# Kernel tuning notes

Measured on AMD Instinct MI355X. Metric: run time of the kernel, lower is better.

## Reference

```python
import jax, jax.numpy as jnp
import numpy as np

N_NODES = 100000
N_EDGES = 1600000
DIM = 128
N_GRAPHS = 64
N_LAYERS = 7
LEAKY_SLOPE = 0.01
BN_EPS = 1e-5


def setup_inputs() -> dict:
    key = jax.random.key(0)
    ks = jax.random.split(key, 6)
    x = jax.random.normal(ks[0], (N_NODES, DIM), dtype=jnp.float32)
    edge_index = jax.random.randint(ks[1], (2, N_EDGES), 0, N_NODES, dtype=jnp.int64)
    batch = jnp.sort(jax.random.randint(ks[2], (N_NODES,), 0, N_GRAPHS, dtype=jnp.int64))
    # GCNConv weights (Glorot-ish scale), biases, BatchNorm affine params
    Ws = jax.random.normal(ks[3], (N_LAYERS, DIM, DIM), dtype=jnp.float32) * (1.0 / np.sqrt(DIM))
    bs = jnp.zeros((N_LAYERS, DIM), dtype=jnp.float32)
    gammas = jnp.ones((N_LAYERS, DIM), dtype=jnp.float32)
    betas = jnp.zeros((N_LAYERS, DIM), dtype=jnp.float32)
    return {"x": x, "edge_index": edge_index, "batch": batch,
            "Ws": Ws, "bs": bs, "gammas": gammas, "betas": betas}


def reference(x, edge_index, batch, Ws, bs, gammas, betas):
    N = x.shape[0]
    # Add self-loops once (shared by all 7 GCNConv layers)
    loops = jnp.arange(N, dtype=edge_index.dtype)
    src = jnp.concatenate([edge_index[0], loops])  # [E+N]
    dst = jnp.concatenate([edge_index[1], loops])  # [E+N]
    # Symmetric normalization: deg over destination (incl. self-loops)
    deg = jax.ops.segment_sum(jnp.ones_like(dst, dtype=x.dtype), dst, num_segments=N)
    dinv = jax.lax.rsqrt(jnp.maximum(deg, 1.0))  # deg >= 1 from self-loops
    norm = dinv[src] * dinv[dst]                 # [E+N]

    def block(h, W, b, gamma, beta):
        # GCNConv: linear -> gather -> normalized scatter-add
        h = h @ W + b                                            # [N, D]
        msgs = h[src] * norm[:, None]                            # [E+N, D]
        h = jax.ops.segment_sum(msgs, dst, num_segments=N)       # [N, D]
        # LeakyReLU then BatchNorm (batch statistics over nodes)
        h = jax.nn.leaky_relu(h, negative_slope=LEAKY_SLOPE)
        mu = jnp.mean(h, axis=0)
        var = jnp.mean((h - mu) ** 2, axis=0)
        h = (h - mu) * jax.lax.rsqrt(var + BN_EPS) * gamma + beta
        return h

    h = x
    for i in range(N_LAYERS):
        h = block(h, Ws[i], bs[i], gammas[i], betas[i])

    # global_mean_pool over graph ids
    sums = jax.ops.segment_sum(h, batch, num_segments=N_GRAPHS)          # [G, D]
    cnt = jax.ops.segment_sum(jnp.ones((N,), h.dtype), batch, num_segments=N_GRAPHS)
    return sums / jnp.maximum(cnt, 1.0)[:, None]
```

## Files before the change

kernel.cpp:

```cpp
#include <hip/hip_runtime.h>
#include <hip/hip_fp16.h>

#define DIMM 128
#define LEAKY_S 0.01f
#define EPS_BN 1e-5f

typedef _Float16 half8 __attribute__((ext_vector_type(8)));
typedef float f32x4 __attribute__((ext_vector_type(4)));


__global__ __launch_bounds__(256) void k_deg(const int* __restrict__ dst, int* __restrict__ deg, int E, int N) {
    int i = blockIdx.x * 256 + threadIdx.x;
    if (i < E) {
        int d = dst[i];
        if ((unsigned)d < (unsigned)N) atomicAdd(&deg[d], 1);
    }
}

__global__ __launch_bounds__(256) void k_dinv(const int* __restrict__ deg, float* __restrict__ dinv, int N) {
    int i = blockIdx.x * 256 + threadIdx.x;
    if (i < N) dinv[i] = rsqrtf((float)(deg[i] + 1));
}

__global__ __launch_bounds__(256) void k_scanA(const int* __restrict__ deg, int* __restrict__ bsum, int n) {
    __shared__ int ws[4];
    int tid = threadIdx.x, lane = tid & 63, wid = tid >> 6;
    int base = blockIdx.x * 1024;
    int s = 0;
    #pragma unroll
    for (int j = 0; j < 4; ++j) {
        int i = base + j * 256 + tid;
        if (i < n) s += deg[i];
    }
    #pragma unroll
    for (int off = 32; off > 0; off >>= 1) s += __shfl_down(s, (unsigned)off, 64);
    if (lane == 0) ws[wid] = s;
    __syncthreads();
    if (tid == 0) bsum[blockIdx.x] = ws[0] + ws[1] + ws[2] + ws[3];
}

__global__ __launch_bounds__(64) void k_scanB(const int* __restrict__ bsum, int* __restrict__ bofs,
                                              int* __restrict__ rowptr, int nb, int n) {
    if (threadIdx.x == 0) {
        int run = 0;
        for (int j = 0; j < nb; ++j) { bofs[j] = run; run += bsum[j]; }
        rowptr[n] = run;
    }
}

__global__ __launch_bounds__(1024) void k_scanC(const int* __restrict__ deg, const int* __restrict__ bofs,
                                                int* __restrict__ rowptr, int n) {
    __shared__ int wsum[16];
    int tid = threadIdx.x, lane = tid & 63, wid = tid >> 6;
    int i = blockIdx.x * 1024 + tid;
    int v = (i < n) ? deg[i] : 0;
    int s = v;
    #pragma unroll
    for (int off = 1; off < 64; off <<= 1) {
        int t = __shfl_up(s, (unsigned)off, 64);
        if (lane >= off) s += t;
    }
    if (lane == 63) wsum[wid] = s;
    __syncthreads();
    if (wid == 0 && lane < 16) {
        int ws = wsum[lane];
        #pragma unroll
        for (int off = 1; off < 16; off <<= 1) {
            int t = __shfl_up(ws, (unsigned)off, 64);
            if (lane >= off) ws += t;
        }
        wsum[lane] = ws;
    }
    __syncthreads();
    int woff = wid ? wsum[wid - 1] : 0;
    if (i < n) rowptr[i] = bofs[blockIdx.x] + woff + (s - v);
}

__global__ __launch_bounds__(256) void k_fill(const int* __restrict__ src, const int* __restrict__ dst,
                                              const int* __restrict__ rowptr, int* __restrict__ cursor,
                                              const float* __restrict__ dinv,
                                              int2* __restrict__ csr, int E, int N) {
    int i = blockIdx.x * 256 + threadIdx.x;
    if (i < E) {
        int d = dst[i], s = src[i];
        if ((unsigned)d < (unsigned)N && (unsigned)s < (unsigned)N) {
            int pos = atomicAdd(&cursor[d], 1);
            int idx = rowptr[d] + pos;
            csr[idx] = make_int2(s, __float_as_int(dinv[s] * dinv[d]));
        }
    }
}


__global__ __launch_bounds__(256) void k_wprep(const float* __restrict__ Ws, __half* __restrict__ Wt) {
    int l = blockIdx.y;
    int i = blockIdx.x * 256 + threadIdx.x;
    int n = i >> 7, k = i & 127;
    Wt[(size_t)l * DIMM * DIMM + n * DIMM + k] = __float2half(Ws[(size_t)l * DIMM * DIMM + k * DIMM + n]);
}


__global__ __launch_bounds__(256) void k_gemm(const void* __restrict__ A, const __half* __restrict__ Wt,
                                              const float* __restrict__ bias, const float* __restrict__ ss,
                                              __half* __restrict__ out, int N, int a_half) {
    __shared__ char smem[128 * 272];
    int tid = threadIdx.x;
    int lane = tid & 63, wid = tid >> 6;
    int quad = lane >> 4, lm = lane & 15;
    int row0 = blockIdx.x * 128;

    {
        int seg = tid & 31;
        int col = seg * 4;
        float4 sc = *(const float4*)(ss + col);
        float4 sh = *(const float4*)(ss + 128 + col);
        const float*  Af = (const float*)A;
        const __half* Ah = (const __half*)A;
        for (int i = tid; i < 128 * 32; i += 256) {
            int r = i >> 5;
            int gr = row0 + r;
            float4 v = make_float4(0.f, 0.f, 0.f, 0.f);
            if (gr < N) {
                if (a_half) {
                    union { uint2 u; __half2 h2[2]; } ld;
                    ld.u = *(const uint2*)(Ah + (size_t)gr * DIMM + col);
                    float2 f0 = __half22float2(ld.h2[0]);
                    float2 f1 = __half22float2(ld.h2[1]);
                    v = make_float4(f0.x, f0.y, f1.x, f1.y);
                } else {
                    v = *(const float4*)(Af + (size_t)gr * DIMM + col);
                }
                v.x = v.x * sc.x + sh.x; v.y = v.y * sc.y + sh.y;
                v.z = v.z * sc.z + sh.z; v.w = v.w * sc.w + sh.w;
            }
            union { _Float16 h[4]; uint2 u; } pk;
            pk.h[0] = (_Float16)v.x; pk.h[1] = (_Float16)v.y;
            pk.h[2] = (_Float16)v.z; pk.h[3] = (_Float16)v.w;
            *(uint2*)(smem + r * 272 + seg * 8) = pk.u;
        }
    }

    f32x4 acc[2][8];
    #pragma unroll
    for (int c = 0; c < 8; ++c) {
        float bc = bias[c * 16 + lm];
        acc[0][c] = (f32x4){bc, bc, bc, bc};
        acc[1][c] = acc[0][c];
    }
    __syncthreads();

    const _Float16* Wt16 = (const _Float16*)Wt;
    #pragma unroll
    for (int kc = 0; kc < 4; ++kc) {
        half8 a0 = *(const half8*)(smem + (wid * 32 + lm) * 272 + kc * 64 + quad * 16);
        half8 a1 = *(const half8*)(smem + (wid * 32 + 16 + lm) * 272 + kc * 64 + quad * 16);
        #pragma unroll
        for (int c = 0; c < 8; ++c) {
            half8 b = *(const half8*)(Wt16 + (c * 16 + lm) * DIMM + kc * 32 + quad * 8);
            acc[0][c] = __builtin_amdgcn_mfma_f32_16x16x32_f16(a0, b, acc[0][c], 0, 0, 0);
            acc[1][c] = __builtin_amdgcn_mfma_f32_16x16x32_f16(a1, b, acc[1][c], 0, 0, 0);
        }
    }

    __syncthreads();
    #pragma unroll
    for (int r = 0; r < 2; ++r)
        #pragma unroll
        for (int c = 0; c < 8; ++c)
            #pragma unroll
            for (int i = 0; i < 4; ++i) {
                int rit = wid * 32 + r * 16 + quad * 4 + i;
                int col = c * 16 + lm;
                *(_Float16*)(smem + rit * 256 + col * 2) = (_Float16)acc[r][c][i];
            }
    __syncthreads();
    for (int i = tid; i < 128 * 16; i += 256) {
        int r = i >> 4, seg = i & 15;
        int gr = row0 + r;
        if (gr < N)
            ((uint4*)(out + (size_t)gr * DIMM))[seg] = ((const uint4*)(smem + r * 256))[seg];
    }
}


__global__ __launch_bounds__(256) void k_agg(const __half* __restrict__ t, __half* __restrict__ out,
                                             const int* __restrict__ rowptr, const int2* __restrict__ csr,
                                             const float* __restrict__ dinv,
                                             float* __restrict__ stats, int N, int nwaves) {
    int tid = threadIdx.x;
    int lane = tid & 63, wid = tid >> 6;
    int grp = lane >> 4;
    int l16 = lane & 15;
    int gw = blockIdx.x * 4 + wid;

    float sx[8] = {0.f, 0.f, 0.f, 0.f, 0.f, 0.f, 0.f, 0.f};
    float qx[8] = {0.f, 0.f, 0.f, 0.f, 0.f, 0.f, 0.f, 0.f};

    for (int node = gw; node < N; node += nwaves) {
        float di = dinv[node];
        float sn = di * di;
        float v[8] = {0.f, 0.f, 0.f, 0.f, 0.f, 0.f, 0.f, 0.f};
        if (grp == 0) {
            union { half8 h; __half2 h2[4]; } u;
            u.h = *(const half8*)(t + (size_t)node * DIMM + l16 * 8);
            #pragma unroll
            for (int p = 0; p < 4; ++p) {
                float2 f = __half22float2(u.h2[p]);
                v[2 * p]     = sn * f.x;
                v[2 * p + 1] = sn * f.y;
            }
        }
        int e = rowptr[node], e1 = rowptr[node + 1];
        for (; e + 16 <= e1; e += 16) {
            #pragma unroll
            for (int j = 0; j < 4; ++j) {
                int2 cw = csr[e + 4 * j + grp];
                float wgt = __int_as_float(cw.y);
                union { half8 h; __half2 h2[4]; } u;
                u.h = *(const half8*)(t + (size_t)cw.x * DIMM + l16 * 8);
                #pragma unroll
                for (int p = 0; p < 4; ++p) {
                    float2 f = __half22float2(u.h2[p]);
                    v[2 * p]     = fmaf(wgt, f.x, v[2 * p]);
                    v[2 * p + 1] = fmaf(wgt, f.y, v[2 * p + 1]);
                }
            }
        }
        if (e < e1) {
            #pragma unroll
            for (int j = 0; j < 4; ++j) {
                int idx = e + 4 * j + grp;
                if (idx < e1) {
                    int2 cw = csr[idx];
                    float wgt = __int_as_float(cw.y);
                    union { half8 h; __half2 h2[4]; } u;
                    u.h = *(const half8*)(t + (size_t)cw.x * DIMM + l16 * 8);
                    #pragma unroll
                    for (int p = 0; p < 4; ++p) {
                        float2 f = __half22float2(u.h2[p]);
                        v[2 * p]     = fmaf(wgt, f.x, v[2 * p]);
                        v[2 * p + 1] = fmaf(wgt, f.y, v[2 * p + 1]);
                    }
                }
            }
        }
        #pragma unroll
        for (int i = 0; i < 8; ++i) {
            v[i] += __shfl_down(v[i], 32, 64);
            v[i] += __shfl_down(v[i], 16, 64);
        }
        if (grp == 0) {
            union { _Float16 h[8]; uint4 u4; } pk;
            #pragma unroll
            for (int i = 0; i < 8; ++i) {
                v[i] = v[i] > 0.f ? v[i] : LEAKY_S * v[i];
                sx[i] += v[i];
                qx[i] += v[i] * v[i];
                pk.h[i] = (_Float16)v[i];
            }
            *(uint4*)(out + (size_t)node * DIMM + l16 * 8) = pk.u4;
        }
    }

    __shared__ float red[4 * 128];
    if (grp == 0) {
        *(float4*)(red + wid * 128 + l16 * 8)     = make_float4(sx[0], sx[1], sx[2], sx[3]);
        *(float4*)(red + wid * 128 + l16 * 8 + 4) = make_float4(sx[4], sx[5], sx[6], sx[7]);
    }
    __syncthreads();
    if (tid < 128) {
        float s = red[tid] + red[128 + tid] + red[256 + tid] + red[384 + tid];
        atomicAdd(&stats[tid], s);
    }
    __syncthreads();
    if (grp == 0) {
        *(float4*)(red + wid * 128 + l16 * 8)     = make_float4(qx[0], qx[1], qx[2], qx[3]);
        *(float4*)(red + wid * 128 + l16 * 8 + 4) = make_float4(qx[4], qx[5], qx[6], qx[7]);
    }
    __syncthreads();
    if (tid < 128) {
        float s = red[tid] + red[128 + tid] + red[256 + tid] + red[384 + tid];
        atomicAdd(&stats[128 + tid], s);
    }
}

__global__ __launch_bounds__(128) void k_bnfin(const float* __restrict__ stats, const float* __restrict__ gamma,
                                               const float* __restrict__ beta, float* __restrict__ ss_out,
                                               float inv_n) {
    int c = threadIdx.x;
    float mu  = stats[c] * inv_n;
    float var = stats[128 + c] * inv_n - mu * mu;
    float a = gamma[c] * rsqrtf(var + EPS_BN);
    ss_out[c]       = a;
    ss_out[128 + c] = beta[c] - mu * a;
}

__global__ __launch_bounds__(128) void k_init_ss(float* __restrict__ ss) {
    int c = threadIdx.x;
    ss[c] = 1.0f;
    ss[128 + c] = 0.0f;
}


__global__ __launch_bounds__(64) void k_cnt_bs(const int* __restrict__ batch, int* __restrict__ cnt, int N, int G) {
    int g = blockIdx.x * 64 + threadIdx.x;
    if (g >= G) return;
    int lo = 0, hi = N;
    while (lo < hi) { int mid = (lo + hi) >> 1; if (batch[mid] < g) lo = mid + 1; else hi = mid; }
    int lb = lo;
    lo = 0; hi = N;
    while (lo < hi) { int mid = (lo + hi) >> 1; if (batch[mid] <= g) lo = mid + 1; else hi = mid; }
    cnt[g] = lo - lb;
}

__global__ __launch_bounds__(128) void k_pool(const __half* __restrict__ h, const int* __restrict__ batch,
                                              float* __restrict__ pool, int N, int G) {
    const int CHUNK = 128;
    int start = blockIdx.x * CHUNK;
    if (start >= N) return;
    int end = min(start + CHUNK, N);
    int tid = threadIdx.x;
    float acc = 0.f;
    int cur = batch[start];
    for (int n = start; n < end; ++n) {
        int g = batch[n];
        if (g != cur) {
            if ((unsigned)cur < (unsigned)G) atomicAdd(&pool[(size_t)cur * DIMM + tid], acc);
            acc = 0.f; cur = g;
        }
        acc += __half2float(h[(size_t)n * DIMM + tid]);
    }
    if ((unsigned)cur < (unsigned)G) atomicAdd(&pool[(size_t)cur * DIMM + tid], acc);
}

__global__ __launch_bounds__(256) void k_poolfin(const float* __restrict__ pool, const int* __restrict__ cnt,
                                                 const float* __restrict__ ss, float* __restrict__ out, int G) {
    int idx = blockIdx.x * 256 + threadIdx.x;
    if (idx < G * DIMM) {
        int g = idx >> 7, c = idx & 127;
        float m = pool[idx] / (float)max(cnt[g], 1);
        out[idx] = ss[c] * m + ss[128 + c];
    }
}


extern "C" void kernel_launch(void* const* d_in, const int* in_sizes, int n_in,
                              void* d_out, int out_size, void* d_ws, size_t ws_size,
                              hipStream_t stream) {
    const float* x      = (const float*)d_in[0];
    const int*   ei     = (const int*)d_in[1];
    const int*   batch  = (const int*)d_in[2];
    const float* Ws     = (const float*)d_in[3];
    const float* bs     = (const float*)d_in[4];
    const float* gammas = (const float*)d_in[5];
    const float* betas  = (const float*)d_in[6];
    float* outp = (float*)d_out;

    int N = in_sizes[2];
    int E = in_sizes[1] / 2;
    int L = in_sizes[3] / (DIMM * DIMM);
    int G = out_size / DIMM;

    const int* srcv = ei;
    const int* dstv = ei + E;

    int nb = (N + 1023) / 1024;

    char* w = (char*)d_ws;
    auto alloc = [&](size_t bytes) { char* p = w; w += (bytes + 511) & ~size_t(511); return p; };
    int*    deg    = (int*)   alloc((size_t)N * 4);
    int*    cursor = (int*)   alloc((size_t)N * 4);
    int*    rowptr = (int*)   alloc((size_t)(N + 1) * 4);
    int*    bsum   = (int*)   alloc((size_t)nb * 4);
    int*    bofs   = (int*)   alloc((size_t)nb * 4);
    int2*   csr    = (int2*)  alloc((size_t)E * 8);
    float*  dinv   = (float*) alloc((size_t)N * 4);
    __half* hA     = (__half*)alloc((size_t)N * DIMM * 2);
    __half* hB     = (__half*)alloc((size_t)N * DIMM * 2);
    __half* Wt     = (__half*)alloc((size_t)L * DIMM * DIMM * 2);
    float*  stats  = (float*) alloc((size_t)L * 256 * 4);
    float*  ss     = (float*) alloc((size_t)(L + 1) * 256 * 4);
    float*  pool   = (float*) alloc((size_t)G * DIMM * 4);
    int*    cnt    = (int*)   alloc((size_t)G * 4);

    hipMemsetAsync(deg,    0, (size_t)N * 4, stream);
    hipMemsetAsync(cursor, 0, (size_t)N * 4, stream);
    hipMemsetAsync(stats,  0, (size_t)L * 256 * 4, stream);
    hipMemsetAsync(pool,   0, (size_t)G * DIMM * 4, stream);

    k_init_ss<<<1, 128, 0, stream>>>(ss);
    k_wprep<<<dim3(64, L), 256, 0, stream>>>(Ws, Wt);
    k_deg  <<<(E + 255) / 256, 256, 0, stream>>>(dstv, deg, E, N);
    k_dinv <<<(N + 255) / 256, 256, 0, stream>>>(deg, dinv, N);
    k_scanA<<<nb, 256, 0, stream>>>(deg, bsum, N);
    k_scanB<<<1, 64, 0, stream>>>(bsum, bofs, rowptr, nb, N);
    k_scanC<<<nb, 1024, 0, stream>>>(deg, bofs, rowptr, N);
    k_fill <<<(E + 255) / 256, 256, 0, stream>>>(srcv, dstv, rowptr, cursor, dinv, csr, E, N);

    const void* cur_in = (const void*)x;
    int a_half = 0;
    for (int l = 0; l < L; ++l) {
        k_gemm<<<(N + 127) / 128, 256, 0, stream>>>(cur_in, Wt + (size_t)l * DIMM * DIMM,
                                                    bs + (size_t)l * DIMM, ss + (size_t)l * 256, hA, N, a_half);
        const int nblk = 2048;
        k_agg<<<nblk, 256, 0, stream>>>(hA, hB, rowptr, csr, dinv,
                                        stats + (size_t)l * 256, N, nblk * 4);
        k_bnfin<<<1, 128, 0, stream>>>(stats + (size_t)l * 256, gammas + (size_t)l * DIMM,
                                       betas + (size_t)l * DIMM, ss + (size_t)(l + 1) * 256, 1.0f / (float)N);
        cur_in = (const void*)hB;
        a_half = 1;
    }

    k_cnt_bs<<<(G + 63) / 64, 64, 0, stream>>>(batch, cnt, N, G);
    k_pool<<<(N + 127) / 128, 128, 0, stream>>>(hB, batch, pool, N, G);
    k_poolfin<<<(G * DIMM + 255) / 256, 256, 0, stream>>>(pool, cnt, ss + (size_t)L * 256, outp, G);
}
```

Baseline: 1.288 ms.

## Slice GEMM output into feature-column planes and aggregate per slice with compact CSR

```diff
diff --git a/kernel.cpp b/kernel.cpp
--- a/kernel.cpp
+++ b/kernel.cpp
@@ -4,9 +4,11 @@
 #define DIMM 128
 #define LEAKY_S 0.01f
 #define EPS_BN 1e-5f
+#define NSLICE 8
 
 typedef _Float16 half8 __attribute__((ext_vector_type(8)));
 typedef float f32x4 __attribute__((ext_vector_type(4)));
+typedef unsigned int uivec4 __attribute__((ext_vector_type(4)));
 
 
 __global__ __launch_bounds__(256) void k_deg(const int* __restrict__ dst, int* __restrict__ deg, int E, int N) {
@@ -17,11 +19,6 @@
     }
 }
 
-__global__ __launch_bounds__(256) void k_dinv(const int* __restrict__ deg, float* __restrict__ dinv, int N) {
-    int i = blockIdx.x * 256 + threadIdx.x;
-    if (i < N) dinv[i] = rsqrtf((float)(deg[i] + 1));
-}
-
 __global__ __launch_bounds__(256) void k_scanA(const int* __restrict__ deg, int* __restrict__ bsum, int n) {
     __shared__ int ws[4];
     int tid = threadIdx.x, lane = tid & 63, wid = tid >> 6;
@@ -30,7 +27,7 @@
     #pragma unroll
     for (int j = 0; j < 4; ++j) {
         int i = base + j * 256 + tid;
-        if (i < n) s += deg[i];
+        if (i < n) s += deg[i] + 1;
     }
     #pragma unroll
     for (int off = 32; off > 0; off >>= 1) s += __shfl_down(s, (unsigned)off, 64);
@@ -53,7 +50,7 @@
     __shared__ int wsum[16];
     int tid = threadIdx.x, lane = tid & 63, wid = tid >> 6;
     int i = blockIdx.x * 1024 + tid;
-    int v = (i < n) ? deg[i] : 0;
+    int v = (i < n) ? deg[i] + 1 : 0;
     int s = v;
     #pragma unroll
     for (int off = 1; off < 64; off <<= 1) {
@@ -76,17 +73,24 @@
     if (i < n) rowptr[i] = bofs[blockIdx.x] + woff + (s - v);
 }
 
+__global__ __launch_bounds__(256) void k_dinvself(const int* __restrict__ deg, const int* __restrict__ rowptr,
+                                                  float* __restrict__ dinv, int* __restrict__ csrcol, int N) {
+    int i = blockIdx.x * 256 + threadIdx.x;
+    if (i < N) {
+        dinv[i] = rsqrtf((float)(deg[i] + 1));
+        csrcol[rowptr[i]] = i;
+    }
+}
+
 __global__ __launch_bounds__(256) void k_fill(const int* __restrict__ src, const int* __restrict__ dst,
                                               const int* __restrict__ rowptr, int* __restrict__ cursor,
-                                              const float* __restrict__ dinv,
-                                              int2* __restrict__ csr, int E, int N) {
+                                              int* __restrict__ csrcol, int E, int N) {
     int i = blockIdx.x * 256 + threadIdx.x;
     if (i < E) {
         int d = dst[i], s = src[i];
         if ((unsigned)d < (unsigned)N && (unsigned)s < (unsigned)N) {
-            int pos = atomicAdd(&cursor[d], 1);
-            int idx = rowptr[d] + pos;
-            csr[idx] = make_int2(s, __float_as_int(dinv[s] * dinv[d]));
+            int pos = 1 + atomicAdd(&cursor[d], 1);
+            csrcol[rowptr[d] + pos] = s;
         }
     }
 }
@@ -174,113 +178,109 @@
                 *(_Float16*)(smem + rit * 256 + col * 2) = (_Float16)acc[r][c][i];
             }
     __syncthreads();
-    for (int i = tid; i < 128 * 16; i += 256) {
-        int r = i >> 4, seg = i & 15;
+    {
+        int r = tid & 127, h = tid >> 7;
         int gr = row0 + r;
-        if (gr < N)
-            ((uint4*)(out + (size_t)gr * DIMM))[seg] = ((const uint4*)(smem + r * 256))[seg];
-    }
-}
-
+        if (gr < N) {
+            #pragma unroll
+            for (int s = 0; s < NSLICE; ++s) {
+                uivec4 val = *(const uivec4*)(smem + r * 256 + s * 32 + h * 16);
+                *(uivec4*)((char*)out + ((size_t)s * N + gr) * 32 + h * 16) = val;
+            }
+        }
+    }
+}
+
+
+__device__ __forceinline__ void h8acc(const __half* p, float w, float* v) {
+    union { uivec4 u; __half2 h2[4]; } ld;
+    ld.u = *(const uivec4*)p;
+    #pragma unroll
+    for (int q = 0; q < 4; ++q) {
+        float2 f = __half22float2(ld.h2[q]);
+        v[2 * q]     = fmaf(w, f.x, v[2 * q]);
+        v[2 * q + 1] = fmaf(w, f.y, v[2 * q + 1]);
+    }
+}
 
 __global__ __launch_bounds__(256) void k_agg(const __half* __restrict__ t, __half* __restrict__ out,
-                                             const int* __restrict__ rowptr, const int2* __restrict__ csr,
+                                             const int* __restrict__ rowptr, const int* __restrict__ csr,
                                              const float* __restrict__ dinv,
-                                             float* __restrict__ stats, int N, int nwaves) {
+                                             float* __restrict__ stats, int N, int stride) {
     int tid = threadIdx.x;
     int lane = tid & 63, wid = tid >> 6;
-    int grp = lane >> 4;
-    int l16 = lane & 15;
-    int gw = blockIdx.x * 4 + wid;
-
-    float sx[8] = {0.f, 0.f, 0.f, 0.f, 0.f, 0.f, 0.f, 0.f};
-    float qx[8] = {0.f, 0.f, 0.f, 0.f, 0.f, 0.f, 0.f, 0.f};
-
-    for (int node = gw; node < N; node += nwaves) {
-        float di = dinv[node];
-        float sn = di * di;
-        float v[8] = {0.f, 0.f, 0.f, 0.f, 0.f, 0.f, 0.f, 0.f};
-        if (grp == 0) {
-            union { half8 h; __half2 h2[4]; } u;
-            u.h = *(const half8*)(t + (size_t)node * DIMM + l16 * 8);
-            #pragma unroll
-            for (int p = 0; p < 4; ++p) {
-                float2 f = __half22float2(u.h2[p]);
-                v[2 * p]     = sn * f.x;
-                v[2 * p + 1] = sn * f.y;
+    int pr = lane >> 1;
+    int half = lane & 1;
+    int s = blockIdx.x & 7;
+    int bs = blockIdx.x >> 3;
+    int gp = bs * 128 + wid * 32 + pr;
+
+    const __half* ts = t + (size_t)s * N * 16;
+
+    float sx[8] = {0.f,0.f,0.f,0.f,0.f,0.f,0.f,0.f};
+    float qx[8] = {0.f,0.f,0.f,0.f,0.f,0.f,0.f,0.f};
+    float acc[8] = {0.f,0.f,0.f,0.f,0.f,0.f,0.f,0.f};
+
+    int node = gp;
+    int e = 0, eend = 0;
+    float dn = 0.f;
+    if (node < N) { e = rowptr[node]; eend = rowptr[node + 1]; dn = dinv[node]; }
+
+    for (;;) {
+        bool act = (node < N);
+        if (__ballot(act) == 0ull) break;
+        int e0 = e;
+        #pragma unroll
+        for (int k = 0; k < 4; ++k) {
+            bool st = act && (e0 + k < eend);
+            if (st) {
+                int col = __builtin_nontemporal_load(csr + e0 + k);
+                float w = dinv[col] * dn;
+                h8acc(ts + (size_t)col * 16 + half * 8, w, acc);
             }
         }
-        int e = rowptr[node], e1 = rowptr[node + 1];
-        for (; e + 16 <= e1; e += 16) {
-            #pragma unroll
-            for (int j = 0; j < 4; ++j) {
-                int2 cw = csr[e + 4 * j + grp];
-                float wgt = __int_as_float(cw.y);
-                union { half8 h; __half2 h2[4]; } u;
-                u.h = *(const half8*)(t + (size_t)cw.x * DIMM + l16 * 8);
+        if (act) {
+            e = min(e0 + 4, eend);
+            if (e >= eend) {
+                union { _Float16 h[8]; uivec4 u4; } pk;
                 #pragma unroll
-                for (int p = 0; p < 4; ++p) {
-                    float2 f = __half22float2(u.h2[p]);
-                    v[2 * p]     = fmaf(wgt, f.x, v[2 * p]);
-                    v[2 * p + 1] = fmaf(wgt, f.y, v[2 * p + 1]);
+                for (int i = 0; i < 8; ++i) {
+                    float v = acc[i];
+                    v = v > 0.f ? v : LEAKY_S * v;
+                    sx[i] += v;
+                    qx[i] += v * v;
+                    pk.h[i] = (_Float16)v;
+                    acc[i] = 0.f;
                 }
+                __builtin_nontemporal_store(pk.u4,
+                    (uivec4*)(out + (size_t)node * DIMM + s * 16 + half * 8));
+                node += stride;
+                if (node < N) { e = rowptr[node]; eend = rowptr[node + 1]; dn = dinv[node]; }
             }
         }
-        if (e < e1) {
-            #pragma unroll
-            for (int j = 0; j < 4; ++j) {
-                int idx = e + 4 * j + grp;
-                if (idx < e1) {
-                    int2 cw = csr[idx];
-                    float wgt = __int_as_float(cw.y);
-                    union { half8 h; __half2 h2[4]; } u;
-                    u.h = *(const half8*)(t + (size_t)cw.x * DIMM + l16 * 8);
-                    #pragma unroll
-                    for (int p = 0; p < 4; ++p) {
-                        float2 f = __half22float2(u.h2[p]);
-                        v[2 * p]     = fmaf(wgt, f.x, v[2 * p]);
-                        v[2 * p + 1] = fmaf(wgt, f.y, v[2 * p + 1]);
-                    }
-                }
-            }
-        }
+    }
+
+    #pragma unroll
+    for (int i = 0; i < 8; ++i) {
+        #pragma unroll
+        for (int d = 2; d <= 32; d <<= 1) {
+            sx[i] += __shfl_down(sx[i], (unsigned)d, 64);
+            qx[i] += __shfl_down(qx[i], (unsigned)d, 64);
+        }
+    }
+    __shared__ float red[4][32];
+    if (lane < 2) {
         #pragma unroll
         for (int i = 0; i < 8; ++i) {
-            v[i] += __shfl_down(v[i], 32, 64);
-            v[i] += __shfl_down(v[i], 16, 64);
-        }
-        if (grp == 0) {
-            union { _Float16 h[8]; uint4 u4; } pk;
-            #pragma unroll
-            for (int i = 0; i < 8; ++i) {
-                v[i] = v[i] > 0.f ? v[i] : LEAKY_S * v[i];
-                sx[i] += v[i];
-                qx[i] += v[i] * v[i];
-                pk.h[i] = (_Float16)v[i];
-            }
-            *(uint4*)(out + (size_t)node * DIMM + l16 * 8) = pk.u4;
-        }
-    }
-
-    __shared__ float red[4 * 128];
-    if (grp == 0) {
-        *(float4*)(red + wid * 128 + l16 * 8)     = make_float4(sx[0], sx[1], sx[2], sx[3]);
-        *(float4*)(red + wid * 128 + l16 * 8 + 4) = make_float4(sx[4], sx[5], sx[6], sx[7]);
-    }
-    __syncthreads();
-    if (tid < 128) {
-        float s = red[tid] + red[128 + tid] + red[256 + tid] + red[384 + tid];
-        atomicAdd(&stats[tid], s);
-    }
-    __syncthreads();
-    if (grp == 0) {
-        *(float4*)(red + wid * 128 + l16 * 8)     = make_float4(qx[0], qx[1], qx[2], qx[3]);
-        *(float4*)(red + wid * 128 + l16 * 8 + 4) = make_float4(qx[4], qx[5], qx[6], qx[7]);
-    }
-    __syncthreads();
-    if (tid < 128) {
-        float s = red[tid] + red[128 + tid] + red[256 + tid] + red[384 + tid];
-        atomicAdd(&stats[128 + tid], s);
+            red[wid][half * 8 + i]      = sx[i];
+            red[wid][16 + half * 8 + i] = qx[i];
+        }
+    }
+    __syncthreads();
+    if (tid < 32) {
+        float v = red[0][tid] + red[1][tid] + red[2][tid] + red[3][tid];
+        int gc = s * 16 + (tid & 15);
+        atomicAdd(&stats[(tid < 16 ? 0 : 128) + gc], v);
     }
 }
 
@@ -373,7 +373,7 @@
     int*    rowptr = (int*)   alloc((size_t)(N + 1) * 4);
     int*    bsum   = (int*)   alloc((size_t)nb * 4);
     int*    bofs   = (int*)   alloc((size_t)nb * 4);
-    int2*   csr    = (int2*)  alloc((size_t)E * 8);
+    int*    csrcol = (int*)   alloc((size_t)(E + N) * 4);
     float*  dinv   = (float*) alloc((size_t)N * 4);
     __half* hA     = (__half*)alloc((size_t)N * DIMM * 2);
     __half* hB     = (__half*)alloc((size_t)N * DIMM * 2);
@@ -383,28 +383,30 @@
     float*  pool   = (float*) alloc((size_t)G * DIMM * 4);
     int*    cnt    = (int*)   alloc((size_t)G * 4);
 
-    hipMemsetAsync(deg,    0, (size_t)N * 4, stream);
-    hipMemsetAsync(cursor, 0, (size_t)N * 4, stream);
-    hipMemsetAsync(stats,  0, (size_t)L * 256 * 4, stream);
-    hipMemsetAsync(pool,   0, (size_t)G * DIMM * 4, stream);
+    (void)hipMemsetAsync(deg,    0, (size_t)N * 4, stream);
+    (void)hipMemsetAsync(cursor, 0, (size_t)N * 4, stream);
+    (void)hipMemsetAsync(stats,  0, (size_t)L * 256 * 4, stream);
+    (void)hipMemsetAsync(pool,   0, (size_t)G * DIMM * 4, stream);
 
     k_init_ss<<<1, 128, 0, stream>>>(ss);
     k_wprep<<<dim3(64, L), 256, 0, stream>>>(Ws, Wt);
     k_deg  <<<(E + 255) / 256, 256, 0, stream>>>(dstv, deg, E, N);
-    k_dinv <<<(N + 255) / 256, 256, 0, stream>>>(deg, dinv, N);
     k_scanA<<<nb, 256, 0, stream>>>(deg, bsum, N);
     k_scanB<<<1, 64, 0, stream>>>(bsum, bofs, rowptr, nb, N);
     k_scanC<<<nb, 1024, 0, stream>>>(deg, bofs, rowptr, N);
-    k_fill <<<(E + 255) / 256, 256, 0, stream>>>(srcv, dstv, rowptr, cursor, dinv, csr, E, N);
+    k_dinvself<<<(N + 255) / 256, 256, 0, stream>>>(deg, rowptr, dinv, csrcol, N);
+    k_fill <<<(E + 255) / 256, 256, 0, stream>>>(srcv, dstv, rowptr, cursor, csrcol, E, N);
+
+    const int nblk = 2048;
+    const int stride = (nblk / NSLICE) * 128;
 
     const void* cur_in = (const void*)x;
     int a_half = 0;
     for (int l = 0; l < L; ++l) {
         k_gemm<<<(N + 127) / 128, 256, 0, stream>>>(cur_in, Wt + (size_t)l * DIMM * DIMM,
                                                     bs + (size_t)l * DIMM, ss + (size_t)l * 256, hA, N, a_half);
-        const int nblk = 2048;
-        k_agg<<<nblk, 256, 0, stream>>>(hA, hB, rowptr, csr, dinv,
-                                        stats + (size_t)l * 256, N, nblk * 4);
+        k_agg<<<nblk, 256, 0, stream>>>(hA, hB, rowptr, csrcol, dinv,
+                                        stats + (size_t)l * 256, N, stride);
         k_bnfin<<<1, 128, 0, stream>>>(stats + (size_t)l * 256, gammas + (size_t)l * DIMM,
                                        betas + (size_t)l * DIMM, ss + (size_t)(l + 1) * 256, 1.0f / (float)N);
         cur_in = (const void*)hB;
```

Result: slower. 2.935 ms (+127.8%).

## Factor symmetric normalization into GEMM epilogue and shrink CSR to column indices

Applied to the files above, without the earlier changes.

```diff
diff --git a/kernel.cpp b/kernel.cpp
--- a/kernel.cpp
+++ b/kernel.cpp
@@ -7,6 +7,7 @@
 
 typedef _Float16 half8 __attribute__((ext_vector_type(8)));
 typedef float f32x4 __attribute__((ext_vector_type(4)));
+typedef unsigned int uivec4 __attribute__((ext_vector_type(4)));
 
 
 __global__ __launch_bounds__(256) void k_deg(const int* __restrict__ dst, int* __restrict__ deg, int E, int N) {
@@ -17,11 +18,6 @@
     }
 }
 
-__global__ __launch_bounds__(256) void k_dinv(const int* __restrict__ deg, float* __restrict__ dinv, int N) {
-    int i = blockIdx.x * 256 + threadIdx.x;
-    if (i < N) dinv[i] = rsqrtf((float)(deg[i] + 1));
-}
-
 __global__ __launch_bounds__(256) void k_scanA(const int* __restrict__ deg, int* __restrict__ bsum, int n) {
     __shared__ int ws[4];
     int tid = threadIdx.x, lane = tid & 63, wid = tid >> 6;
@@ -30,7 +26,7 @@
     #pragma unroll
     for (int j = 0; j < 4; ++j) {
         int i = base + j * 256 + tid;
-        if (i < n) s += deg[i];
+        if (i < n) s += deg[i] + 1;
     }
     #pragma unroll
     for (int off = 32; off > 0; off >>= 1) s += __shfl_down(s, (unsigned)off, 64);
@@ -53,7 +49,7 @@
     __shared__ int wsum[16];
     int tid = threadIdx.x, lane = tid & 63, wid = tid >> 6;
     int i = blockIdx.x * 1024 + tid;
-    int v = (i < n) ? deg[i] : 0;
+    int v = (i < n) ? deg[i] + 1 : 0;
     int s = v;
     #pragma unroll
     for (int off = 1; off < 64; off <<= 1) {
@@ -76,17 +72,24 @@
     if (i < n) rowptr[i] = bofs[blockIdx.x] + woff + (s - v);
 }
 
+__global__ __launch_bounds__(256) void k_dinvself(const int* __restrict__ deg, const int* __restrict__ rowptr,
+                                                  float* __restrict__ dinv, int* __restrict__ csrcol, int N) {
+    int i = blockIdx.x * 256 + threadIdx.x;
+    if (i < N) {
+        dinv[i] = rsqrtf((float)(deg[i] + 1));
+        csrcol[rowptr[i]] = i;
+    }
+}
+
 __global__ __launch_bounds__(256) void k_fill(const int* __restrict__ src, const int* __restrict__ dst,
                                               const int* __restrict__ rowptr, int* __restrict__ cursor,
-                                              const float* __restrict__ dinv,
-                                              int2* __restrict__ csr, int E, int N) {
+                                              int* __restrict__ csrcol, int E, int N) {
     int i = blockIdx.x * 256 + threadIdx.x;
     if (i < E) {
         int d = dst[i], s = src[i];
         if ((unsigned)d < (unsigned)N && (unsigned)s < (unsigned)N) {
-            int pos = atomicAdd(&cursor[d], 1);
-            int idx = rowptr[d] + pos;
-            csr[idx] = make_int2(s, __float_as_int(dinv[s] * dinv[d]));
+            int pos = 1 + atomicAdd(&cursor[d], 1);
+            csrcol[rowptr[d] + pos] = s;
         }
     }
 }
@@ -102,6 +105,7 @@
 
 __global__ __launch_bounds__(256) void k_gemm(const void* __restrict__ A, const __half* __restrict__ Wt,
                                               const float* __restrict__ bias, const float* __restrict__ ss,
+                                              const float* __restrict__ dinv,
                                               __half* __restrict__ out, int N, int a_half) {
     __shared__ char smem[128 * 272];
     int tid = threadIdx.x;
@@ -162,6 +166,15 @@
         }
     }
 
+    float dv[2][4];
+    #pragma unroll
+    for (int r = 0; r < 2; ++r)
+        #pragma unroll
+        for (int i = 0; i < 4; ++i) {
+            int gr = row0 + wid * 32 + r * 16 + quad * 4 + i;
+            dv[r][i] = (gr < N) ? dinv[gr] : 0.f;
+        }
+
     __syncthreads();
     #pragma unroll
     for (int r = 0; r < 2; ++r)
@@ -171,20 +184,31 @@
             for (int i = 0; i < 4; ++i) {
                 int rit = wid * 32 + r * 16 + quad * 4 + i;
                 int col = c * 16 + lm;
-                *(_Float16*)(smem + rit * 256 + col * 2) = (_Float16)acc[r][c][i];
+                *(_Float16*)(smem + rit * 256 + col * 2) = (_Float16)(acc[r][c][i] * dv[r][i]);
             }
     __syncthreads();
     for (int i = tid; i < 128 * 16; i += 256) {
         int r = i >> 4, seg = i & 15;
         int gr = row0 + r;
         if (gr < N)
-            ((uint4*)(out + (size_t)gr * DIMM))[seg] = ((const uint4*)(smem + r * 256))[seg];
-    }
-}
-
+            ((uivec4*)(out + (size_t)gr * DIMM))[seg] = ((const uivec4*)(smem + r * 256))[seg];
+    }
+}
+
+
+__device__ __forceinline__ void h8add(const __half* p, float* v) {
+    union { uivec4 u; __half2 h2[4]; } ld;
+    ld.u = *(const uivec4*)p;
+    #pragma unroll
+    for (int q = 0; q < 4; ++q) {
+        float2 f = __half22float2(ld.h2[q]);
+        v[2 * q]     += f.x;
+        v[2 * q + 1] += f.y;
+    }
+}
 
 __global__ __launch_bounds__(256) void k_agg(const __half* __restrict__ t, __half* __restrict__ out,
-                                             const int* __restrict__ rowptr, const int2* __restrict__ csr,
+                                             const int* __restrict__ rowptr, const int* __restrict__ csr,
                                              const float* __restrict__ dinv,
                                              float* __restrict__ stats, int N, int nwaves) {
     int tid = threadIdx.x;
@@ -193,37 +217,18 @@
     int l16 = lane & 15;
     int gw = blockIdx.x * 4 + wid;
 
-    float sx[8] = {0.f, 0.f, 0.f, 0.f, 0.f, 0.f, 0.f, 0.f};
-    float qx[8] = {0.f, 0.f, 0.f, 0.f, 0.f, 0.f, 0.f, 0.f};
+    float sx[8] = {0.f,0.f,0.f,0.f,0.f,0.f,0.f,0.f};
+    float qx[8] = {0.f,0.f,0.f,0.f,0.f,0.f,0.f,0.f};
 
     for (int node = gw; node < N; node += nwaves) {
-        float di = dinv[node];
-        float sn = di * di;
-        float v[8] = {0.f, 0.f, 0.f, 0.f, 0.f, 0.f, 0.f, 0.f};
-        if (grp == 0) {
-            union { half8 h; __half2 h2[4]; } u;
-            u.h = *(const half8*)(t + (size_t)node * DIMM + l16 * 8);
-            #pragma unroll
-            for (int p = 0; p < 4; ++p) {
-                float2 f = __half22float2(u.h2[p]);
-                v[2 * p]     = sn * f.x;
-                v[2 * p + 1] = sn * f.y;
-            }
-        }
+        float dn = dinv[node];
+        float v[8] = {0.f,0.f,0.f,0.f,0.f,0.f,0.f,0.f};
         int e = rowptr[node], e1 = rowptr[node + 1];
         for (; e + 16 <= e1; e += 16) {
             #pragma unroll
             for (int j = 0; j < 4; ++j) {
-                int2 cw = csr[e + 4 * j + grp];
-                float wgt = __int_as_float(cw.y);
-                union { half8 h; __half2 h2[4]; } u;
-                u.h = *(const half8*)(t + (size_t)cw.x * DIMM + l16 * 8);
-                #pragma unroll
-                for (int p = 0; p < 4; ++p) {
-                    float2 f = __half22float2(u.h2[p]);
-                    v[2 * p]     = fmaf(wgt, f.x, v[2 * p]);
-                    v[2 * p + 1] = fmaf(wgt, f.y, v[2 * p + 1]);
-                }
+                int col = __builtin_nontemporal_load(csr + e + 4 * j + grp);
+                h8add(t + (size_t)col * DIMM + l16 * 8, v);
             }
         }
         if (e < e1) {
@@ -231,16 +236,8 @@
             for (int j = 0; j < 4; ++j) {
                 int idx = e + 4 * j + grp;
                 if (idx < e1) {
-                    int2 cw = csr[idx];
-                    float wgt = __int_as_float(cw.y);
-                    union { half8 h; __half2 h2[4]; } u;
-                    u.h = *(const half8*)(t + (size_t)cw.x * DIMM + l16 * 8);
-                    #pragma unroll
-                    for (int p = 0; p < 4; ++p) {
-                        float2 f = __half22float2(u.h2[p]);
-                        v[2 * p]     = fmaf(wgt, f.x, v[2 * p]);
-                        v[2 * p + 1] = fmaf(wgt, f.y, v[2 * p + 1]);
-                    }
+                    int col = __builtin_nontemporal_load(csr + idx);
+                    h8add(t + (size_t)col * DIMM + l16 * 8, v);
                 }
             }
         }
@@ -250,15 +247,16 @@
             v[i] += __shfl_down(v[i], 16, 64);
         }
         if (grp == 0) {
-            union { _Float16 h[8]; uint4 u4; } pk;
+            union { _Float16 h[8]; uivec4 u4; } pk;
             #pragma unroll
             for (int i = 0; i < 8; ++i) {
-                v[i] = v[i] > 0.f ? v[i] : LEAKY_S * v[i];
-                sx[i] += v[i];
-                qx[i] += v[i] * v[i];
-                pk.h[i] = (_Float16)v[i];
+                float w = dn * v[i];
+                w = w > 0.f ? w : LEAKY_S * w;
+                sx[i] += w;
+                qx[i] += w * w;
+                pk.h[i] = (_Float16)w;
             }
-            *(uint4*)(out + (size_t)node * DIMM + l16 * 8) = pk.u4;
+            *(uivec4*)(out + (size_t)node * DIMM + l16 * 8) = pk.u4;
         }
     }
 
@@ -373,7 +371,7 @@
     int*    rowptr = (int*)   alloc((size_t)(N + 1) * 4);
     int*    bsum   = (int*)   alloc((size_t)nb * 4);
     int*    bofs   = (int*)   alloc((size_t)nb * 4);
-    int2*   csr    = (int2*)  alloc((size_t)E * 8);
+    int*    csrcol = (int*)   alloc((size_t)(E + N) * 4);
     float*  dinv   = (float*) alloc((size_t)N * 4);
     __half* hA     = (__half*)alloc((size_t)N * DIMM * 2);
     __half* hB     = (__half*)alloc((size_t)N * DIMM * 2);
@@ -383,27 +381,28 @@
     float*  pool   = (float*) alloc((size_t)G * DIMM * 4);
     int*    cnt    = (int*)   alloc((size_t)G * 4);
 
-    hipMemsetAsync(deg,    0, (size_t)N * 4, stream);
-    hipMemsetAsync(cursor, 0, (size_t)N * 4, stream);
-    hipMemsetAsync(stats,  0, (size_t)L * 256 * 4, stream);
-    hipMemsetAsync(pool,   0, (size_t)G * DIMM * 4, stream);
+    (void)hipMemsetAsync(deg,    0, (size_t)N * 4, stream);
+    (void)hipMemsetAsync(cursor, 0, (size_t)N * 4, stream);
+    (void)hipMemsetAsync(stats,  0, (size_t)L * 256 * 4, stream);
+    (void)hipMemsetAsync(pool,   0, (size_t)G * DIMM * 4, stream);
 
     k_init_ss<<<1, 128, 0, stream>>>(ss);
     k_wprep<<<dim3(64, L), 256, 0, stream>>>(Ws, Wt);
     k_deg  <<<(E + 255) / 256, 256, 0, stream>>>(dstv, deg, E, N);
-    k_dinv <<<(N + 255) / 256, 256, 0, stream>>>(deg, dinv, N);
     k_scanA<<<nb, 256, 0, stream>>>(deg, bsum, N);
     k_scanB<<<1, 64, 0, stream>>>(bsum, bofs, rowptr, nb, N);
     k_scanC<<<nb, 1024, 0, stream>>>(deg, bofs, rowptr, N);
-    k_fill <<<(E + 255) / 256, 256, 0, stream>>>(srcv, dstv, rowptr, cursor, dinv, csr, E, N);
+    k_dinvself<<<(N + 255) / 256, 256, 0, stream>>>(deg, rowptr, dinv, csrcol, N);
+    k_fill <<<(E + 255) / 256, 256, 0, stream>>>(srcv, dstv, rowptr, cursor, csrcol, E, N);
 
     const void* cur_in = (const void*)x;
     int a_half = 0;
     for (int l = 0; l < L; ++l) {
         k_gemm<<<(N + 127) / 128, 256, 0, stream>>>(cur_in, Wt + (size_t)l * DIMM * DIMM,
-                                                    bs + (size_t)l * DIMM, ss + (size_t)l * 256, hA, N, a_half);
+                                                    bs + (size_t)l * DIMM, ss + (size_t)l * 256,
+                                                    dinv, hA, N, a_half);
         const int nblk = 2048;
-        k_agg<<<nblk, 256, 0, stream>>>(hA, hB, rowptr, csr, dinv,
+        k_agg<<<nblk, 256, 0, stream>>>(hA, hB, rowptr, csrcol, dinv,
                                         stats + (size_t)l * 256, N, nblk * 4);
         k_bnfin<<<1, 128, 0, stream>>>(stats + (size_t)l * 256, gammas + (size_t)l * DIMM,
                                        betas + (size_t)l * DIMM, ss + (size_t)(l + 1) * 256, 1.0f / (float)N);
```

Result: slower. 1.378 ms (+7.0%).
